# Kernel optimization log

Measured on AMD Instinct MI355X. Metric: run time of the kernel, lower is better.

## Reference

```python
import jax, jax.numpy as jnp
import numpy as np

B, C, H, W = 16, 256, 64, 64

def setup_inputs() -> dict:
    key = jax.random.key(0)
    ks = jax.random.split(key, 4)
    scale = 1.0 / np.sqrt(C)
    return {
        "x": jax.random.normal(ks[0], (B, C, H, W), dtype=jnp.float32),
        "w1": jax.random.normal(ks[1], (C, C), dtype=jnp.float32) * scale,
        "b1": jnp.zeros((C,), dtype=jnp.float32),
        "w2": jax.random.normal(ks[2], (C, C), dtype=jnp.float32) * scale,
        "b2": jnp.zeros((C,), dtype=jnp.float32),
        "w3": jax.random.normal(ks[3], (C, C), dtype=jnp.float32) * scale,
        "b3": jnp.zeros((C,), dtype=jnp.float32),
    }

def reference(x, w1, b1, w2, b2, w3, b3):
    b, c, h, w = x.shape
    n = h * w
    # 1x1 convs == per-pixel linear maps over channels; w has shape [C_out, C_in]
    def proj(wt, bias):
        return jnp.einsum('bchw,oc->bohw', x, wt) + bias[None, :, None, None]
    v = proj(w1, b1).reshape(b, c, n).transpose(0, 2, 1)   # [B, N, C]
    q = proj(w2, b2).reshape(b, c, n)                      # [B, C, N]
    k = proj(w3, b3).reshape(b, c, n)                      # [B, C, N]
    weight = jnp.einsum('bcn,bdn->bcd', q, k)              # [B, C, C]
    # global softmax over the entire flattened C*C matrix per batch element
    weight = jax.nn.softmax(weight.reshape(b, -1), axis=1).reshape(b, c, c)
    out = jnp.einsum('bnc,bcd->bdn', v, weight)            # [B, C, N]
    return out.reshape(x.shape)
```

## Files before the change

### kernel.cpp

```cpp
#include <hip/hip_runtime.h>


typedef unsigned short u16;
typedef __attribute__((ext_vector_type(8))) short short8;
typedef __attribute__((ext_vector_type(4))) float floatx4;

__device__ __forceinline__ u16 f2b(float f) {
  union { float f; unsigned int u; } v; v.f = f;
  unsigned int u = v.u;
  return (u16)((u + 0x7fffu + ((u >> 16) & 1u)) >> 16);
}
__device__ __forceinline__ float b2f(u16 h) {
  union { unsigned int u; float f; } v; v.u = ((unsigned int)h) << 16;
  return v.f;
}
__device__ __forceinline__ unsigned int cvt_pk_bf16(float lo, float hi) {
  unsigned int r;
  asm("v_cvt_pk_bf16_f32 %0, %1, %2" : "=v"(r) : "v"(lo), "v"(hi));
  return r;
}
__device__ __forceinline__ void gload_lds16(const u16* g, u16* l) {
  __builtin_amdgcn_global_load_lds(
      (const __attribute__((address_space(1))) unsigned int*)(const void*)g,
      (__attribute__((address_space(3))) unsigned int*)(void*)l, 16, 0, 0);
}

__global__ __launch_bounds__(256) void prep_w_kernel(
    const float* __restrict__ w1, const float* __restrict__ w2, const float* __restrict__ w3,
    u16* __restrict__ W1Th, u16* __restrict__ W2h, u16* __restrict__ W2l,
    u16* __restrict__ W3h, u16* __restrict__ W3l, float* __restrict__ xsum) {
  const int blk = blockIdx.x, t = threadIdx.x;
  if (blk == 576) {
#pragma unroll
    for (int i = 0; i < 16; ++i) xsum[t + i * 256] = 0.f;
    return;
  }
  if (blk < 64) {
    __shared__ float tile[32][33];
    const int e0 = (blk & 7) * 32, c0 = (blk >> 3) * 32;
    const int tx = t & 31, ty = t >> 5;
#pragma unroll
    for (int i = 0; i < 4; ++i)
      tile[ty + i * 8][tx] = w1[(c0 + ty + i * 8) * 256 + e0 + tx];
    __syncthreads();
#pragma unroll
    for (int i = 0; i < 4; ++i)
      W1Th[(e0 + ty + i * 8) * 256 + c0 + tx] = f2b(tile[tx][ty + i * 8]);
  } else {
    const int i = (blk - 64) * 256 + t;
    const int e = i & 0xffff;
    const float f = (i >> 16) ? w3[e] : w2[e];
    u16 h = f2b(f);
    if (i >> 16) { W3h[e] = h; W3l[e] = f2b(f - b2f(h)); }
    else         { W2h[e] = h; W2l[e] = f2b(f - b2f(h)); }
  }
}

__device__ __forceinline__ void stage8(const float4 a, const float4 b,
                                       u16* dH, u16* dL, float& xa) {
  const float f[8] = {a.x, a.y, a.z, a.w, b.x, b.y, b.z, b.w};
  union { unsigned int w[4]; uint4 q; } uh, ul;
#pragma unroll
  for (int i = 0; i < 4; ++i) {
    const unsigned int h = cvt_pk_bf16(f[2 * i], f[2 * i + 1]);
    uh.w[i] = h;
    union { unsigned int u; float ff; } h0, h1;
    h0.u = h << 16;
    h1.u = h & 0xffff0000u;
    ul.w[i] = cvt_pk_bf16(f[2 * i] - h0.ff, f[2 * i + 1] - h1.ff);
    xa += f[2 * i] + f[2 * i + 1];
  }
  *(uint4*)dH = uh.q;
  *(uint4*)dL = ul.q;
}

__global__ __launch_bounds__(512, 4) void gram_kernel(
    const float* __restrict__ x, float* __restrict__ Gp, float* __restrict__ xsum) {
  __shared__ u16 lH[2][256 * 32], lL[2][256 * 32];
  const int b = blockIdx.x >> 5, s = (blockIdx.x >> 1) & 15, mh = blockIdx.x & 1;
  const float* Xb = x + (long)b * 1048576 + s * 256;
  const int t = threadIdx.x;
  const int lane = t & 63, wave = t >> 6;
  const int quad = lane >> 4, l16 = lane & 15;
  const int wml = (wave & 1) * 64 + mh * 128;
  const int wn = (wave >> 1) * 64;
  const int r0 = t >> 2, qc = (t & 3) * 8;
  const int r1 = r0 + 128;
  const int wq = (((t & 3) ^ ((r0 >> 1) & 3))) * 8;
  const int rq = ((quad ^ ((l16 >> 1) & 3))) * 8;
  floatx4 acc[4][4] = {};
  float xa0 = 0.f, xa1 = 0.f;
  float4 p[4];
  p[0] = *(const float4*)(Xb + (long)r0 * 4096 + qc);
  p[1] = *(const float4*)(Xb + (long)r0 * 4096 + qc + 4);
  p[2] = *(const float4*)(Xb + (long)r1 * 4096 + qc);
  p[3] = *(const float4*)(Xb + (long)r1 * 4096 + qc + 4);
  stage8(p[0], p[1], lH[0] + r0 * 32 + wq, lL[0] + r0 * 32 + wq, xa0);
  stage8(p[2], p[3], lH[0] + r1 * 32 + wq, lL[0] + r1 * 32 + wq, xa1);
  __syncthreads();
  for (int kb = 0; kb < 8; ++kb) {
    const int cur = kb & 1, nxt = cur ^ 1;
    if (kb < 7) {
      const long kk = (kb + 1) * 32;
      p[0] = *(const float4*)(Xb + (long)r0 * 4096 + kk + qc);
      p[1] = *(const float4*)(Xb + (long)r0 * 4096 + kk + qc + 4);
      p[2] = *(const float4*)(Xb + (long)r1 * 4096 + kk + qc);
      p[3] = *(const float4*)(Xb + (long)r1 * 4096 + kk + qc + 4);
    }
    const u16* cH = lH[cur];
    const u16* cL = lL[cur];
    short8 ah[4], al[4];
#pragma unroll
    for (int i = 0; i < 4; ++i) {
      ah[i] = *(const short8*)(cH + (wml + i * 16 + l16) * 32 + rq);
      al[i] = *(const short8*)(cL + (wml + i * 16 + l16) * 32 + rq);
    }
#pragma unroll
    for (int j = 0; j < 4; ++j) {
      const short8 bh = *(const short8*)(cH + (wn + j * 16 + l16) * 32 + rq);
      const short8 bl = *(const short8*)(cL + (wn + j * 16 + l16) * 32 + rq);
#pragma unroll
      for (int i = 0; i < 4; ++i) {
        acc[i][j] = __builtin_amdgcn_mfma_f32_16x16x32_bf16(ah[i], bh, acc[i][j], 0, 0, 0);
        acc[i][j] = __builtin_amdgcn_mfma_f32_16x16x32_bf16(ah[i], bl, acc[i][j], 0, 0, 0);
        acc[i][j] = __builtin_amdgcn_mfma_f32_16x16x32_bf16(al[i], bh, acc[i][j], 0, 0, 0);
      }
    }
    if (kb < 7) {
      stage8(p[0], p[1], lH[nxt] + r0 * 32 + wq, lL[nxt] + r0 * 32 + wq, xa0);
      stage8(p[2], p[3], lH[nxt] + r1 * 32 + wq, lL[nxt] + r1 * 32 + wq, xa1);
    }
    __syncthreads();
  }
  if (mh == 0) {
    float v = xa0;
    v += __shfl_xor(v, 1);
    v += __shfl_xor(v, 2);
    if ((t & 3) == 0) atomicAdd(&xsum[b * 256 + r0], v);
    v = xa1;
    v += __shfl_xor(v, 1);
    v += __shfl_xor(v, 2);
    if ((t & 3) == 0) atomicAdd(&xsum[b * 256 + r1], v);
  }
  float* G = Gp + ((long)b * 16 + s) * 65536;
#pragma unroll
  for (int i = 0; i < 4; ++i) {
    const int row0 = wml + i * 16 + quad * 4;
#pragma unroll
    for (int j = 0; j < 4; ++j) {
      const int col = wn + j * 16 + l16;
#pragma unroll
      for (int r = 0; r < 4; ++r)
        G[(long)(row0 + r) * 256 + col] = acc[i][j][r];
    }
  }
}

__global__ __launch_bounds__(256) void reduce_g_kernel(
    const float* __restrict__ Gp, u16* __restrict__ Gh, u16* __restrict__ Gl) {
  const long e = ((long)blockIdx.x * 256 + threadIdx.x) * 4;
  const long base = ((e >> 16) << 20) + (e & 65535);
  float4 s = {0.f, 0.f, 0.f, 0.f};
#pragma unroll
  for (int i = 0; i < 16; ++i) {
    const float4 v = *(const float4*)(Gp + base + (long)i * 65536);
    s.x += v.x; s.y += v.y; s.z += v.z; s.w += v.w;
  }
  union { u16 h[4]; uint2 q; } oh, ol;
  const float sv[4] = {s.x, s.y, s.z, s.w};
#pragma unroll
  for (int c = 0; c < 4; ++c) {
    const u16 h = f2b(sv[c]);
    oh.h[c] = h;
    ol.h[c] = f2b(sv[c] - b2f(h));
  }
  *(uint2*)(Gh + e) = oh.q;
  *(uint2*)(Gl + e) = ol.q;
}

template <bool X3, int EPI>
__global__ __launch_bounds__(256) void gemm_small(
    const u16* __restrict__ Ah, const u16* __restrict__ Al,
    const u16* __restrict__ Bh, const u16* __restrict__ Bl,
    long aBatch, long bBatch, long oBatch,
    float* __restrict__ outF, u16* __restrict__ outH, u16* __restrict__ outL) {
  constexpr int LR = 40;
  __shared__ u16 smem[(X3 ? 4 : 2) * 64 * LR];
  u16* lAh = smem;
  u16* lBh = smem + 64 * LR;
  u16* lAl = X3 ? (smem + 2 * 64 * LR) : nullptr;
  u16* lBl = X3 ? (smem + 3 * 64 * LR) : nullptr;
  const int b = blockIdx.z;
  const int tm = blockIdx.x & 3, tn = blockIdx.x >> 2;
  const u16* Ahb = Ah + (long)b * aBatch + (long)tm * 64 * 256;
  const u16* Bhb = Bh + (long)b * bBatch + (long)tn * 64 * 256;
  const u16* Alb = X3 ? (Al + (long)b * aBatch + (long)tm * 64 * 256) : nullptr;
  const u16* Blb = X3 ? (Bl + (long)b * bBatch + (long)tn * 64 * 256) : nullptr;
  const int t = threadIdx.x;
  const int lane = t & 63, wave = t >> 6;
  const int quad = lane >> 4, l16 = lane & 15;
  const int wm = (wave & 1) * 32, wn = (wave >> 1) * 32;
  const int r = t >> 2, qc = (t & 3) * 8;
  floatx4 acc[2][2] = {};
  uint4 pA, pB, pAl = {}, pBl = {};
  pA = *(const uint4*)(Ahb + (long)r * 256 + qc);
  pB = *(const uint4*)(Bhb + (long)r * 256 + qc);
  if (X3) {
    pAl = *(const uint4*)(Alb + (long)r * 256 + qc);
    pBl = *(const uint4*)(Blb + (long)r * 256 + qc);
  }
  for (int kk = 0; kk < 256; kk += 32) {
    __syncthreads();
    *(uint4*)(lAh + r * LR + qc) = pA;
    *(uint4*)(lBh + r * LR + qc) = pB;
    if (X3) {
      *(uint4*)(lAl + r * LR + qc) = pAl;
      *(uint4*)(lBl + r * LR + qc) = pBl;
    }
    __syncthreads();
    if (kk < 224) {
      pA = *(const uint4*)(Ahb + (long)r * 256 + kk + 32 + qc);
      pB = *(const uint4*)(Bhb + (long)r * 256 + kk + 32 + qc);
      if (X3) {
        pAl = *(const uint4*)(Alb + (long)r * 256 + kk + 32 + qc);
        pBl = *(const uint4*)(Blb + (long)r * 256 + kk + 32 + qc);
      }
    }
    short8 afh[2], bfh[2], afl[2], bfl[2];
#pragma unroll
    for (int i = 0; i < 2; ++i) {
      afh[i] = *(const short8*)(lAh + (wm + i * 16 + l16) * LR + quad * 8);
      bfh[i] = *(const short8*)(lBh + (wn + i * 16 + l16) * LR + quad * 8);
      if (X3) {
        afl[i] = *(const short8*)(lAl + (wm + i * 16 + l16) * LR + quad * 8);
        bfl[i] = *(const short8*)(lBl + (wn + i * 16 + l16) * LR + quad * 8);
      }
    }
#pragma unroll
    for (int i = 0; i < 2; ++i)
#pragma unroll
      for (int j = 0; j < 2; ++j) {
        acc[i][j] = __builtin_amdgcn_mfma_f32_16x16x32_bf16(afh[i], bfh[j], acc[i][j], 0, 0, 0);
        if (X3) {
          acc[i][j] = __builtin_amdgcn_mfma_f32_16x16x32_bf16(afh[i], bfl[j], acc[i][j], 0, 0, 0);
          acc[i][j] = __builtin_amdgcn_mfma_f32_16x16x32_bf16(afl[i], bfh[j], acc[i][j], 0, 0, 0);
        }
      }
  }
  const long obase = (long)b * oBatch;
#pragma unroll
  for (int i = 0; i < 2; ++i) {
    const int mb = tm * 64 + wm + i * 16 + quad * 4;
#pragma unroll
    for (int j = 0; j < 2; ++j) {
      const int n = tn * 64 + wn + j * 16 + l16;
#pragma unroll
      for (int rr = 0; rr < 4; ++rr) {
        const float v = acc[i][j][rr];
        const long idx = obase + (long)(mb + rr) * 256 + n;
        if (EPI == 0) {
          outF[idx] = v;
        } else if (EPI == 1) {
          u16 h = f2b(v);
          outH[idx] = h;
          outL[idx] = f2b(v - b2f(h));
        } else {
          outH[idx] = f2b(v);
        }
      }
    }
  }
}

__global__ __launch_bounds__(512, 2) void gemm_out(
    const u16* __restrict__ Mh, const float* __restrict__ x,
    const float* __restrict__ bb, float* __restrict__ out) {
  __shared__ u16 lA[2][256 * 32];
  __shared__ u16 lB[128 * 40];
  const int b = blockIdx.z;
  const int tn = blockIdx.x;
  const u16* Ab = Mh + (long)b * 65536;
  const float* Xb = x + (long)b * 1048576 + tn * 128;
  const int t = threadIdx.x;
  const int lane = t & 63, wave = t >> 6;
  const int quad = lane >> 4, l16 = lane & 15;
  const int wm = (wave & 3) * 64;
  const int wn = (wave >> 2) * 64;
  const int erp = (t >> 5) * 2;
  const int n0 = t & 31;
  const int ra = t >> 2;
  const int sc = ((t & 3) ^ ((t >> 3) & 3)) * 8;
  const int rqA = (quad ^ ((l16 >> 1) & 3)) * 8;
  u16* wA0 = &lA[0][0] + wave * 16 * 32;
  u16* wA1 = &lA[1][0] + wave * 16 * 32;
  floatx4 acc[4][4] = {};
  float pb[8];
  gload_lds16(Ab + (long)ra * 256 + sc, wA0);
  gload_lds16(Ab + (long)(ra + 128) * 256 + sc, wA0 + 128 * 32);
#pragma unroll
  for (int i = 0; i < 4; ++i) {
    pb[i]     = Xb[(long)erp * 4096 + n0 + 32 * i];
    pb[4 + i] = Xb[(long)(erp + 1) * 4096 + n0 + 32 * i];
  }
  for (int s = 0; s < 8; ++s) {
    const int kk = s * 32;
    const u16* curA = lA[s & 1];
    __syncthreads();
#pragma unroll
    for (int i = 0; i < 4; ++i) {
      const int nl = n0 + 32 * i;
      const int sb = (erp >> 3) ^ ((nl >> 4) & 3);
      *(unsigned int*)(lB + nl * 40 + sb * 8 + (erp & 7)) =
          cvt_pk_bf16(pb[i], pb[4 + i]);
    }
    __syncthreads();
    if (s < 7) {
      const int k2 = kk + 32;
      u16* nA = (s & 1) ? wA0 : wA1;
      gload_lds16(Ab + (long)ra * 256 + k2 + sc, nA);
      gload_lds16(Ab + (long)(ra + 128) * 256 + k2 + sc, nA + 128 * 32);
#pragma unroll
      for (int i = 0; i < 4; ++i) {
        pb[i]     = Xb[(long)(k2 + erp) * 4096 + n0 + 32 * i];
        pb[4 + i] = Xb[(long)(k2 + erp + 1) * 4096 + n0 + 32 * i];
      }
    }
    short8 af[4];
#pragma unroll
    for (int i = 0; i < 4; ++i)
      af[i] = *(const short8*)(curA + (wm + i * 16 + l16) * 32 + rqA);
#pragma unroll
    for (int j = 0; j < 4; ++j) {
      const int n = wn + j * 16 + l16;
      const int rb = quad ^ ((n >> 4) & 3);
      const short8 bf = *(const short8*)(lB + n * 40 + rb * 8);
#pragma unroll
      for (int i = 0; i < 4; ++i)
        acc[i][j] = __builtin_amdgcn_mfma_f32_16x16x32_bf16(af[i], bf, acc[i][j], 0, 0, 0);
    }
  }
  const long obase = (long)b * 1048576;
#pragma unroll
  for (int i = 0; i < 4; ++i) {
    const int mb = wm + i * 16 + quad * 4;
#pragma unroll
    for (int j = 0; j < 4; ++j) {
      const int n = tn * 128 + wn + j * 16 + l16;
#pragma unroll
      for (int r = 0; r < 4; ++r)
        out[obase + (long)(mb + r) * 4096 + n] = acc[i][j][r] + bb[b * 256 + mb + r];
    }
  }
}

__global__ __launch_bounds__(512) void bias_prep_kernel(
    const float* __restrict__ w2, const float* __restrict__ w3,
    const float* __restrict__ xsum, float* __restrict__ S2, float* __restrict__ S3) {
  __shared__ float xs[256];
  const int b = blockIdx.x, t = threadIdx.x;
  if (t < 256) xs[t] = xsum[b * 256 + t];
  __syncthreads();
  const float* wm = (t < 256) ? w2 : w3;
  const int a = t & 255;
  float s = 0.f;
#pragma unroll 4
  for (int c = 0; c < 256; ++c) s += wm[a * 256 + c] * xs[c];
  if (t < 256) S2[b * 256 + a] = s;
  else         S3[b * 256 + a] = s;
}

__global__ __launch_bounds__(256) void softmax_pass1(
    const float* __restrict__ Lt, const float* __restrict__ S2, const float* __restrict__ S3,
    const float* __restrict__ b2, const float* __restrict__ b3,
    float* __restrict__ bm, float* __restrict__ bs) {
  __shared__ float ls2[256], lb2[256];
  __shared__ float redm[4], reds[4];
  const int b = blockIdx.y, blk = blockIdx.x, t = threadIdx.x;
  ls2[t] = S2[b * 256 + t];
  lb2[t] = b2[t];
  __syncthreads();
  const int fw0 = blk * 2048 + t * 8;
  const int d = fw0 >> 8, a0 = fw0 & 255;
  const float c1 = b3[d];
  const float c0 = S3[b * 256 + d] + 4096.f * c1;
  const long base = (long)b * 65536 + fw0;
  float4 v0 = *(const float4*)(Lt + base);
  float4 v1 = *(const float4*)(Lt + base + 4);
  float v[8] = {v0.x, v0.y, v0.z, v0.w, v1.x, v1.y, v1.z, v1.w};
  float m = -3.4e38f;
#pragma unroll
  for (int i = 0; i < 8; ++i) {
    v[i] += lb2[a0 + i] * c0 + c1 * ls2[a0 + i];
    m = fmaxf(m, v[i]);
  }
  for (int o = 32; o; o >>= 1) m = fmaxf(m, __shfl_xor(m, o));
  const int wid = t >> 6, lane = t & 63;
  if (lane == 0) redm[wid] = m;
  __syncthreads();
  const float bmax = fmaxf(fmaxf(redm[0], redm[1]), fmaxf(redm[2], redm[3]));
  float s = 0.f;
#pragma unroll
  for (int i = 0; i < 8; ++i) s += __expf(v[i] - bmax);
  for (int o = 32; o; o >>= 1) s += __shfl_xor(s, o);
  if (lane == 0) reds[wid] = s;
  __syncthreads();
  if (t == 0) {
    bm[b * 32 + blk] = bmax;
    bs[b * 32 + blk] = reds[0] + reds[1] + reds[2] + reds[3];
  }
}

__global__ __launch_bounds__(256) void softmax_pass3(
    const float* __restrict__ Lt, const float* __restrict__ S2, const float* __restrict__ S3,
    const float* __restrict__ b2, const float* __restrict__ b3,
    const float* __restrict__ bm, const float* __restrict__ bs,
    const float* __restrict__ b1, u16* __restrict__ WTh, float* __restrict__ bb) {
  __shared__ float ls2[256], lb2[256], lb1[256];
  __shared__ float sM, sInv;
  const int b = blockIdx.y, blk = blockIdx.x, t = threadIdx.x;
  if (t < 64) {
    const float m = (t < 32) ? bm[b * 32 + t] : -3.4e38f;
    float s = (t < 32) ? bs[b * 32 + t] : 0.f;
    float M = m;
    for (int o = 32; o; o >>= 1) M = fmaxf(M, __shfl_xor(M, o));
    s *= __expf(m - M);
    for (int o = 32; o; o >>= 1) s += __shfl_xor(s, o);
    if (t == 0) { sM = M; sInv = 1.0f / s; }
  }
  ls2[t] = S2[b * 256 + t];
  lb2[t] = b2[t];
  lb1[t] = b1[t];
  __syncthreads();
  const float M = sM, inv = sInv;
  const int fw0 = blk * 2048 + t * 8;
  const int d = fw0 >> 8, a0 = fw0 & 255;
  const float c1 = b3[d];
  const float c0 = S3[b * 256 + d] + 4096.f * c1;
  const long base = (long)b * 65536 + fw0;
  float4 v0 = *(const float4*)(Lt + base);
  float4 v1 = *(const float4*)(Lt + base + 4);
  float v[8] = {v0.x, v0.y, v0.z, v0.w, v1.x, v1.y, v1.z, v1.w};
  union { u16 h[8]; uint4 q; } o;
  float bsum = 0.f;
#pragma unroll
  for (int i = 0; i < 8; ++i) {
    const float vv = v[i] + lb2[a0 + i] * c0 + c1 * ls2[a0 + i];
    const float w = __expf(vv - M) * inv;
    o.h[i] = f2b(w);
    bsum += w * lb1[a0 + i];
  }
  *(uint4*)(WTh + base) = o.q;
  for (int off = 16; off; off >>= 1) bsum += __shfl_xor(bsum, off);
  if ((t & 31) == 0) bb[b * 256 + d] = bsum;
}

extern "C" void kernel_launch(void* const* d_in, const int* in_sizes, int n_in,
                              void* d_out, int out_size, void* d_ws, size_t ws_size,
                              hipStream_t stream) {
  const float* x  = (const float*)d_in[0];
  const float* w1 = (const float*)d_in[1];
  const float* b1 = (const float*)d_in[2];
  const float* w2 = (const float*)d_in[3];
  const float* b2 = (const float*)d_in[4];
  const float* w3 = (const float*)d_in[5];
  const float* b3 = (const float*)d_in[6];
  float* out = (float*)d_out;

  char* ws = (char*)d_ws;
  size_t off = 0;
  auto alloc = [&](size_t bytes) {
    void* p = ws + off;
    off += (bytes + 255) & ~(size_t)255;
    return p;
  };
  float* Gp = (float*)alloc(16ull * 16 * 65536 * 4);
  float* xsum = (float*)alloc(16 * 256 * 4);
  u16* Gh   = (u16*)alloc(16ull * 65536 * 2);
  u16* Gl   = (u16*)alloc(16ull * 65536 * 2);
  u16* T3h  = (u16*)alloc(16ull * 65536 * 2);
  u16* T3l  = (u16*)alloc(16ull * 65536 * 2);
  float* Lb = (float*)alloc(16ull * 65536 * 4);
  u16* WTh  = (u16*)alloc(16ull * 65536 * 2);
  u16* Mh   = (u16*)alloc(16ull * 65536 * 2);
  u16* W1Th = (u16*)alloc(65536 * 2);
  u16* W2h  = (u16*)alloc(65536 * 2);
  u16* W2l  = (u16*)alloc(65536 * 2);
  u16* W3h  = (u16*)alloc(65536 * 2);
  u16* W3l  = (u16*)alloc(65536 * 2);
  float* S2   = (float*)alloc(16 * 256 * 4);
  float* S3   = (float*)alloc(16 * 256 * 4);
  float* bmx  = (float*)alloc(16 * 32 * 4);
  float* bsx  = (float*)alloc(16 * 32 * 4);
  float* bb   = (float*)alloc(16 * 256 * 4);

  prep_w_kernel<<<577, 256, 0, stream>>>(w1, w2, w3, W1Th, W2h, W2l, W3h, W3l, xsum);

  gram_kernel<<<512, 512, 0, stream>>>(x, Gp, xsum);
  reduce_g_kernel<<<1024, 256, 0, stream>>>(Gp, Gh, Gl);

  gemm_small<true, 1><<<dim3(16, 1, 16), 256, 0, stream>>>(
      W3h, W3l, Gh, Gl, 0, 65536, 65536, nullptr, T3h, T3l);
  gemm_small<true, 0><<<dim3(16, 1, 16), 256, 0, stream>>>(
      T3h, T3l, W2h, W2l, 65536, 0, 65536, Lb, nullptr, nullptr);

  bias_prep_kernel<<<16, 512, 0, stream>>>(w2, w3, xsum, S2, S3);
  softmax_pass1<<<dim3(32, 16), 256, 0, stream>>>(Lb, S2, S3, b2, b3, bmx, bsx);
  softmax_pass3<<<dim3(32, 16), 256, 0, stream>>>(Lb, S2, S3, b2, b3, bmx, bsx,
                                                  b1, WTh, bb);

  gemm_small<false, 2><<<dim3(16, 1, 16), 256, 0, stream>>>(
      WTh, nullptr, W1Th, nullptr, 65536, 0, 65536, nullptr, Mh, nullptr);
  gemm_out<<<dim3(32, 1, 16), 512, 0, stream>>>(Mh, x, bb, out);
}
```

Measured before the change: 218.4 us.

## Load full K=256 tiles into LDS once instead of streaming K-chunks

gemm_small now loads the entire 64x256 A and B tiles (and the low-half tiles in X3 mode) into shared memory up front with a single barrier. The K loop then runs fully unrolled out of LDS, with no per-iteration barriers or register prefetch. This removes the sixteen synchronisations per block and lets the global loads issue back to back. In exchange, LDS use grows to about 67 KB in X3 mode, which cuts occupancy, and no global loads overlap with MFMA work.

```diff
diff --git a/kernel.cpp b/kernel.cpp
--- a/kernel.cpp
+++ b/kernel.cpp
@@ -184,68 +184,85 @@
     const u16* __restrict__ Bh, const u16* __restrict__ Bl,
     long aBatch, long bBatch, long oBatch,
     float* __restrict__ outF, u16* __restrict__ outH, u16* __restrict__ outL) {
-  constexpr int LR = 40;
-  __shared__ u16 smem[(X3 ? 4 : 2) * 64 * LR];
+  constexpr int LW = 264;
+  __shared__ u16 smem[(X3 ? 4 : 2) * 64 * LW];
   u16* lAh = smem;
-  u16* lBh = smem + 64 * LR;
-  u16* lAl = X3 ? (smem + 2 * 64 * LR) : nullptr;
-  u16* lBl = X3 ? (smem + 3 * 64 * LR) : nullptr;
+  u16* lBh = smem + 64 * LW;
+  u16* lAl = X3 ? (smem + 2 * 64 * LW) : nullptr;
+  u16* lBl = X3 ? (smem + 3 * 64 * LW) : nullptr;
   const int b = blockIdx.z;
   const int tm = blockIdx.x & 3, tn = blockIdx.x >> 2;
   const u16* Ahb = Ah + (long)b * aBatch + (long)tm * 64 * 256;
   const u16* Bhb = Bh + (long)b * bBatch + (long)tn * 64 * 256;
-  const u16* Alb = X3 ? (Al + (long)b * aBatch + (long)tm * 64 * 256) : nullptr;
-  const u16* Blb = X3 ? (Bl + (long)b * bBatch + (long)tn * 64 * 256) : nullptr;
   const int t = threadIdx.x;
   const int lane = t & 63, wave = t >> 6;
   const int quad = lane >> 4, l16 = lane & 15;
   const int wm = (wave & 1) * 32, wn = (wave >> 1) * 32;
-  const int r = t >> 2, qc = (t & 3) * 8;
+  const int r = t >> 2, c4 = t & 3;
+  {
+    uint4 tmp[8];
+#pragma unroll
+    for (int j = 0; j < 8; ++j)
+      tmp[j] = *(const uint4*)(Ahb + (long)r * 256 + (c4 + 4 * j) * 8);
+#pragma unroll
+    for (int j = 0; j < 8; ++j)
+      *(uint4*)(lAh + r * LW + (c4 + 4 * j) * 8) = tmp[j];
+#pragma unroll
+    for (int j = 0; j < 8; ++j)
+      tmp[j] = *(const uint4*)(Bhb + (long)r * 256 + (c4 + 4 * j) * 8);
+#pragma unroll
+    for (int j = 0; j < 8; ++j)
+      *(uint4*)(lBh + r * LW + (c4 + 4 * j) * 8) = tmp[j];
+    if (X3) {
+      const u16* Alb = Al + (long)b * aBatch + (long)tm * 64 * 256;
+      const u16* Blb = Bl + (long)b * bBatch + (long)tn * 64 * 256;
+#pragma unroll
+      for (int j = 0; j < 8; ++j)
+        tmp[j] = *(const uint4*)(Alb + (long)r * 256 + (c4 + 4 * j) * 8);
+#pragma unroll
+      for (int j = 0; j < 8; ++j)
+        *(uint4*)(lAl + r * LW + (c4 + 4 * j) * 8) = tmp[j];
+#pragma unroll
+      for (int j = 0; j < 8; ++j)
+        tmp[j] = *(const uint4*)(Blb + (long)r * 256 + (c4 + 4 * j) * 8);
+#pragma unroll
+      for (int j = 0; j < 8; ++j)
+        *(uint4*)(lBl + r * LW + (c4 + 4 * j) * 8) = tmp[j];
+    }
+  }
+  __syncthreads();
   floatx4 acc[2][2] = {};
-  uint4 pA, pB, pAl = {}, pBl = {};
-  pA = *(const uint4*)(Ahb + (long)r * 256 + qc);
-  pB = *(const uint4*)(Bhb + (long)r * 256 + qc);
-  if (X3) {
-    pAl = *(const uint4*)(Alb + (long)r * 256 + qc);
-    pBl = *(const uint4*)(Blb + (long)r * 256 + qc);
-  }
-  for (int kk = 0; kk < 256; kk += 32) {
-    __syncthreads();
-    *(uint4*)(lAh + r * LR + qc) = pA;
-    *(uint4*)(lBh + r * LR + qc) = pB;
+#pragma unroll
+  for (int kk = 0; kk < 8; ++kk) {
+    const int co = kk * 32 + quad * 8;
+    short8 afh[2], bfh[2];
+#pragma unroll
+    for (int i = 0; i < 2; ++i) {
+      afh[i] = *(const short8*)(lAh + (wm + i * 16 + l16) * LW + co);
+      bfh[i] = *(const short8*)(lBh + (wn + i * 16 + l16) * LW + co);
+    }
     if (X3) {
-      *(uint4*)(lAl + r * LR + qc) = pAl;
-      *(uint4*)(lBl + r * LR + qc) = pBl;
-    }
-    __syncthreads();
-    if (kk < 224) {
-      pA = *(const uint4*)(Ahb + (long)r * 256 + kk + 32 + qc);
-      pB = *(const uint4*)(Bhb + (long)r * 256 + kk + 32 + qc);
-      if (X3) {
-        pAl = *(const uint4*)(Alb + (long)r * 256 + kk + 32 + qc);
-        pBl = *(const uint4*)(Blb + (long)r * 256 + kk + 32 + qc);
+      short8 afl[2], bfl[2];
+#pragma unroll
+      for (int i = 0; i < 2; ++i) {
+        afl[i] = *(const short8*)(lAl + (wm + i * 16 + l16) * LW + co);
+        bfl[i] = *(const short8*)(lBl + (wn + i * 16 + l16) * LW + co);
       }
-    }
-    short8 afh[2], bfh[2], afl[2], bfl[2];
-#pragma unroll
-    for (int i = 0; i < 2; ++i) {
-      afh[i] = *(const short8*)(lAh + (wm + i * 16 + l16) * LR + quad * 8);
-      bfh[i] = *(const short8*)(lBh + (wn + i * 16 + l16) * LR + quad * 8);
-      if (X3) {
-        afl[i] = *(const short8*)(lAl + (wm + i * 16 + l16) * LR + quad * 8);
-        bfl[i] = *(const short8*)(lBl + (wn + i * 16 + l16) * LR + quad * 8);
-      }
-    }
-#pragma unroll
-    for (int i = 0; i < 2; ++i)
-#pragma unroll
-      for (int j = 0; j < 2; ++j) {
-        acc[i][j] = __builtin_amdgcn_mfma_f32_16x16x32_bf16(afh[i], bfh[j], acc[i][j], 0, 0, 0);
-        if (X3) {
+#pragma unroll
+      for (int i = 0; i < 2; ++i)
+#pragma unroll
+        for (int j = 0; j < 2; ++j) {
+          acc[i][j] = __builtin_amdgcn_mfma_f32_16x16x32_bf16(afh[i], bfh[j], acc[i][j], 0, 0, 0);
           acc[i][j] = __builtin_amdgcn_mfma_f32_16x16x32_bf16(afh[i], bfl[j], acc[i][j], 0, 0, 0);
           acc[i][j] = __builtin_amdgcn_mfma_f32_16x16x32_bf16(afl[i], bfh[j], acc[i][j], 0, 0, 0);
         }
-      }
+    } else {
+#pragma unroll
+      for (int i = 0; i < 2; ++i)
+#pragma unroll
+        for (int j = 0; j < 2; ++j)
+          acc[i][j] = __builtin_amdgcn_mfma_f32_16x16x32_bf16(afh[i], bfh[j], acc[i][j], 0, 0, 0);
+    }
   }
   const long obase = (long)b * oBatch;
 #pragma unroll
```

Result: no change. 217.1 us (-0.6%).
